# Performance work log

Measured on AMD Instinct MI355X. Metric: run time of the kernel, lower is better.

## Reference

```python
import jax, jax.numpy as jnp
import numpy as np

B, N, C, H = 2, 2048, 1024, 16
D = C // H  # head dim = 64


def setup_inputs() -> dict:
    key = jax.random.key(0)
    k1, k2, k3 = jax.random.split(key, 3)
    x = jax.random.normal(k1, (B, N, C), dtype=jnp.float32)
    w_qkv = jax.random.normal(k2, (C, 3 * C), dtype=jnp.float32) * 0.02
    w_proj = jax.random.normal(k3, (C, C), dtype=jnp.float32) * 0.02
    b_proj = jnp.zeros((C,), dtype=jnp.float32)
    return {"x": x, "w_qkv": w_qkv, "w_proj": w_proj, "b_proj": b_proj}


def reference(x, w_qkv, w_proj, b_proj):
    Bx, Nx, Cx = x.shape
    h, d = H, Cx // H
    # fused QKV projection (no bias: qkv_bias=False)
    qkv = x @ w_qkv  # [B, N, 3C]
    qkv = qkv.reshape(Bx, Nx, 3, h, d).transpose(2, 0, 3, 1, 4)  # [3, B, H, N, D]
    q, k, v = qkv[0], qkv[1], qkv[2]
    # scaled dot-product attention weights (full NxN matrix, as in flax)
    scale = jnp.asarray(1.0 / np.sqrt(d), dtype=x.dtype)
    scores = jnp.einsum('bhqd,bhkd->bhqk', q * scale, k)  # [B, H, N, N]
    attn = jax.nn.softmax(scores, axis=-1)
    # attention-value matmul, merge heads
    out = jnp.einsum('bhqk,bhkd->bhqd', attn, v)  # [B, H, N, D]
    out = out.swapaxes(1, 2).reshape(Bx, Nx, Cx)  # [B, N, C]
    # output projection (with bias: use_bias=True)
    return out @ w_proj + b_proj
```

## Files before the change

### kernel.cpp

```cpp
#include <hip/hip_runtime.h>
#include <cstdint>
#include <cstddef>

#define B_ 2
#define N_ 2048
#define C_ 1024
#define H_ 16

typedef unsigned short u16;
typedef __attribute__((ext_vector_type(8))) short bf16x8;
typedef __attribute__((ext_vector_type(4))) float f32x4;
typedef __attribute__((ext_vector_type(8))) u16 u16x8;
typedef __attribute__((ext_vector_type(4))) u16 u16x4;

static __device__ __forceinline__ u16 f2bf(float f) {
  unsigned int u = __builtin_bit_cast(unsigned int, f);
  u += 0x7FFFu + ((u >> 16) & 1u);
  return (u16)(u >> 16);
}

__global__ void cvt_f32_bf16(const float* __restrict__ in, u16* __restrict__ out) {
  const size_t i = (size_t)(blockIdx.x * blockDim.x + threadIdx.x) * 4;
  const float4 v = *(const float4*)(in + i);
  u16x4 o;
  o[0] = f2bf(v.x); o[1] = f2bf(v.y); o[2] = f2bf(v.z); o[3] = f2bf(v.w);
  *(u16x4*)(out + i) = o;
}

__global__ void tcvt_bf16(const float* __restrict__ in, u16* __restrict__ out,
                          int R, int Cn) {
  __shared__ float T[32][33];
  const int t = threadIdx.x;
  const int c0 = blockIdx.x * 32, r0 = blockIdx.y * 32;
  {
    const int r = t >> 3, c4 = (t & 7) * 4;
    const float4 v = *(const float4*)(in + (size_t)(r0 + r) * Cn + c0 + c4);
    T[r][c4 + 0] = v.x; T[r][c4 + 1] = v.y; T[r][c4 + 2] = v.z; T[r][c4 + 3] = v.w;
  }
  __syncthreads();
  {
    const int c = t >> 3, r4 = (t & 7) * 4;
    u16x4 o;
    o[0] = f2bf(T[r4 + 0][c]); o[1] = f2bf(T[r4 + 1][c]);
    o[2] = f2bf(T[r4 + 2][c]); o[3] = f2bf(T[r4 + 3][c]);
    *(u16x4*)(out + (size_t)(c0 + c) * R + r0 + r4) = o;
  }
}

__global__ __launch_bounds__(256, 4)
void vtrans(const u16* __restrict__ qkv, u16* __restrict__ vt) {
  __shared__ u16 T[64][72];
  const int tid = threadIdx.x;
  const int bh = blockIdx.x, tile = blockIdx.y;
  const int b = bh >> 4, h = bh & 15;
  const size_t src = (size_t)(b * N_ + tile * 64) * 3072 + 2048 + h * 64;
#pragma unroll
  for (int i = 0; i < 2; ++i) {
    const int f = tid + i * 256;
    const int row = f >> 3, d8 = (f & 7) * 8;
    *(u16x8*)&T[row][d8] = *(const u16x8*)(qkv + src + (size_t)row * 3072 + d8);
  }
  __syncthreads();
#pragma unroll
  for (int i = 0; i < 2; ++i) {
    const int f = tid + i * 256;
    const int d = f >> 3, n8 = (f & 7) * 8;
    u16x8 o;
#pragma unroll
    for (int j = 0; j < 8; ++j) o[j] = T[n8 + j][d];
    *(u16x8*)(vt + (size_t)(bh * 64 + d) * N_ + tile * 64 + n8) = o;
  }
}

template<bool BIAS, bool OUTBF>
__global__ __launch_bounds__(256, 2)
void gemm_bf16(const u16* __restrict__ A, const u16* __restrict__ Bt,
               const float* __restrict__ bias, float* __restrict__ Cf,
               u16* __restrict__ Cb, int M, int Nn, int K)
{
  __shared__ u16 As[128][40];
  __shared__ u16 Bs[128][40];

  const int tid = threadIdx.x;
  const int lane = tid & 63, wv = tid >> 6;
  const int wr = wv >> 1, wc = wv & 1;
  const int lr = lane & 15, lk = (lane >> 4) * 8;

  f32x4 acc[4][4];
#pragma unroll
  for (int m = 0; m < 4; ++m)
#pragma unroll
    for (int n = 0; n < 4; ++n) acc[m][n] = (f32x4){0.f, 0.f, 0.f, 0.f};

  const u16* Ag = A + (size_t)(blockIdx.y * 128) * K;
  const u16* Bg = Bt + (size_t)(blockIdx.x * 128) * K;

  for (int kt = 0; kt < K; kt += 32) {
#pragma unroll
    for (int i = 0; i < 2; ++i) {
      const int f = tid + i * 256;
      const int row = f >> 2, kq = (f & 3) * 8;
      *(u16x8*)&As[row][kq] = *(const u16x8*)(Ag + (size_t)row * K + kt + kq);
      *(u16x8*)&Bs[row][kq] = *(const u16x8*)(Bg + (size_t)row * K + kt + kq);
    }
    __syncthreads();

    bf16x8 a[4], b[4];
#pragma unroll
    for (int m = 0; m < 4; ++m) a[m] = *(bf16x8*)&As[wr * 64 + m * 16 + lr][lk];
#pragma unroll
    for (int n = 0; n < 4; ++n) b[n] = *(bf16x8*)&Bs[wc * 64 + n * 16 + lr][lk];
#pragma unroll
    for (int m = 0; m < 4; ++m)
#pragma unroll
      for (int n = 0; n < 4; ++n)
        acc[m][n] = __builtin_amdgcn_mfma_f32_16x16x32_bf16(a[m], b[n], acc[m][n], 0, 0, 0);
    __syncthreads();
  }

#pragma unroll
  for (int n = 0; n < 4; ++n) {
    const int col = blockIdx.x * 128 + wc * 64 + n * 16 + lr;
    const float bv = BIAS ? bias[col] : 0.f;
#pragma unroll
    for (int m = 0; m < 4; ++m) {
      const int rbase = blockIdx.y * 128 + wr * 64 + m * 16 + (lane >> 4) * 4;
#pragma unroll
      for (int r = 0; r < 4; ++r) {
        if (OUTBF) Cb[(size_t)(rbase + r) * Nn + col] = f2bf(acc[m][n][r]);
        else       Cf[(size_t)(rbase + r) * Nn + col] = acc[m][n][r] + bv;
      }
    }
  }
}

__global__ __launch_bounds__(256, 3)
void attn_mfma(const u16* __restrict__ qkv, const u16* __restrict__ vt,
               u16* __restrict__ att)
{
  __shared__ u16 Ks[64][72];
  __shared__ u16 Vs[64][72];
  __shared__ u16 Ps[64][72];

  const int tid = threadIdx.x;
  const int lane = tid & 63, wv = tid >> 6;
  const int l15 = lane & 15, lg = lane >> 4;
  const int qt = blockIdx.x;
  const int bh = blockIdx.y;
  const int b = bh >> 4, h = bh & 15;

  const size_t qbase = (size_t)(b * N_ + qt * 64) * 3072 + h * 64;
  const size_t kcol  = (size_t)b * N_ * 3072 + 1024 + h * 64;
  const size_t vbase = (size_t)(bh * 64) * N_;

#pragma unroll
  for (int i = 0; i < 2; ++i) {
    const int f = tid + i * 256;
    const int row = f >> 3, d8 = (f & 7) * 8;
    *(u16x8*)&Ps[row][d8] = *(const u16x8*)(qkv + qbase + (size_t)row * 3072 + d8);
  }
  __syncthreads();
  bf16x8 qf[2];
#pragma unroll
  for (int ks = 0; ks < 2; ++ks) qf[ks] = *(bf16x8*)&Ps[wv * 16 + l15][ks * 32 + lg * 8];
  __syncthreads();

  f32x4 accO[4];
#pragma unroll
  for (int n = 0; n < 4; ++n) accO[n] = (f32x4){0.f, 0.f, 0.f, 0.f};
  float m[4] = {-INFINITY, -INFINITY, -INFINITY, -INFINITY};
  float l[4] = {0.f, 0.f, 0.f, 0.f};

  for (int t = 0; t < N_ / 64; ++t) {
#pragma unroll
    for (int i = 0; i < 2; ++i) {
      const int f = tid + i * 256;
      const int row = f >> 3, c8 = (f & 7) * 8;
      *(u16x8*)&Ks[row][c8] =
          *(const u16x8*)(qkv + kcol + (size_t)(t * 64 + row) * 3072 + c8);
      *(u16x8*)&Vs[row][c8] =
          *(const u16x8*)(vt + vbase + (size_t)row * N_ + t * 64 + c8);
    }
    __syncthreads();

    f32x4 s[4];
#pragma unroll
    for (int n = 0; n < 4; ++n) {
      s[n] = (f32x4){0.f, 0.f, 0.f, 0.f};
#pragma unroll
      for (int ks = 0; ks < 2; ++ks) {
        const bf16x8 kf = *(bf16x8*)&Ks[n * 16 + l15][ks * 32 + lg * 8];
        s[n] = __builtin_amdgcn_mfma_f32_16x16x32_bf16(qf[ks], kf, s[n], 0, 0, 0);
      }
    }

    float mx[4], scf[4], ps[4];
#pragma unroll
    for (int n = 0; n < 4; ++n)
#pragma unroll
      for (int r = 0; r < 4; ++r) s[n][r] *= 0.125f;
#pragma unroll
    for (int r = 0; r < 4; ++r)
      mx[r] = fmaxf(fmaxf(s[0][r], s[1][r]), fmaxf(s[2][r], s[3][r]));
#pragma unroll
    for (int mask = 1; mask < 16; mask <<= 1)
#pragma unroll
      for (int r = 0; r < 4; ++r) mx[r] = fmaxf(mx[r], __shfl_xor(mx[r], mask));
#pragma unroll
    for (int r = 0; r < 4; ++r) {
      const float mn = fmaxf(m[r], mx[r]);
      scf[r] = __expf(m[r] - mn);
      m[r] = mn;
      ps[r] = 0.f;
    }
#pragma unroll
    for (int n = 0; n < 4; ++n)
#pragma unroll
      for (int r = 0; r < 4; ++r) {
        const float p = __expf(s[n][r] - m[r]);
        s[n][r] = p;
        ps[r] += p;
      }
#pragma unroll
    for (int mask = 1; mask < 16; mask <<= 1)
#pragma unroll
      for (int r = 0; r < 4; ++r) ps[r] += __shfl_xor(ps[r], mask);
#pragma unroll
    for (int r = 0; r < 4; ++r) l[r] = l[r] * scf[r] + ps[r];
#pragma unroll
    for (int n = 0; n < 4; ++n)
#pragma unroll
      for (int r = 0; r < 4; ++r) accO[n][r] *= scf[r];

#pragma unroll
    for (int n = 0; n < 4; ++n)
#pragma unroll
      for (int r = 0; r < 4; ++r)
        Ps[wv * 16 + lg * 4 + r][n * 16 + l15] = f2bf(s[n][r]);

#pragma unroll
    for (int ks = 0; ks < 2; ++ks) {
      const bf16x8 pa = *(bf16x8*)&Ps[wv * 16 + l15][ks * 32 + lg * 8];
#pragma unroll
      for (int n = 0; n < 4; ++n) {
        const bf16x8 vf = *(bf16x8*)&Vs[n * 16 + l15][ks * 32 + lg * 8];
        accO[n] = __builtin_amdgcn_mfma_f32_16x16x32_bf16(pa, vf, accO[n], 0, 0, 0);
      }
    }
    __syncthreads();
  }

  float inv[4];
#pragma unroll
  for (int r = 0; r < 4; ++r) inv[r] = 1.f / l[r];
#pragma unroll
  for (int n = 0; n < 4; ++n) {
    const int col = h * 64 + n * 16 + l15;
#pragma unroll
    for (int r = 0; r < 4; ++r) {
      const int row = b * N_ + qt * 64 + wv * 16 + lg * 4 + r;
      att[(size_t)row * C_ + col] = f2bf(accO[n][r] * inv[r]);
    }
  }
}

extern "C" void kernel_launch(void* const* d_in, const int* in_sizes, int n_in,
                              void* d_out, int out_size, void* d_ws, size_t ws_size,
                              hipStream_t stream) {
  const float* x      = (const float*)d_in[0];
  const float* w_qkv  = (const float*)d_in[1];
  const float* w_proj = (const float*)d_in[2];
  const float* b_proj = (const float*)d_in[3];
  float* out = (float*)d_out;

  u16* qkvb = (u16*)d_ws;
  u16* xb   = qkvb + (size_t)4096 * 3072;
  u16* wqt  = xb   + (size_t)4096 * 1024;
  u16* wpt  = wqt  + (size_t)3072 * 1024;
  u16* aob  = wpt  + (size_t)1024 * 1024;
  u16* vt   = xb;

  const int M = B_ * N_;

  cvt_f32_bf16<<<4096, 256, 0, stream>>>(x, xb);
  tcvt_bf16<<<dim3(96, 32), 256, 0, stream>>>(w_qkv, wqt, C_, 3 * C_);
  tcvt_bf16<<<dim3(32, 32), 256, 0, stream>>>(w_proj, wpt, C_, C_);

  gemm_bf16<false, true><<<dim3(3 * C_ / 128, M / 128), 256, 0, stream>>>(
      xb, wqt, nullptr, nullptr, qkvb, M, 3 * C_, C_);

  vtrans<<<dim3(32, 32), 256, 0, stream>>>(qkvb, vt);

  attn_mfma<<<dim3(N_ / 64, B_ * H_), 256, 0, stream>>>(qkvb, vt, aob);

  gemm_bf16<true, false><<<dim3(C_ / 128, M / 128), 256, 0, stream>>>(
      aob, wpt, b_proj, out, nullptr, M, C_, C_);
}
```

Baseline: 277.2 us.

## Double-buffer K/V tiles in attention and swizzle blocks for XCD locality

```diff
diff --git a/kernel.cpp b/kernel.cpp
--- a/kernel.cpp
+++ b/kernel.cpp
@@ -138,27 +138,32 @@
 void attn_mfma(const u16* __restrict__ qkv, const u16* __restrict__ vt,
                u16* __restrict__ att)
 {
-  __shared__ u16 Ks[64][72];
-  __shared__ u16 Vs[64][72];
+  __shared__ u16 Ks[2][64][72];
+  __shared__ u16 Vs[2][64][72];
   __shared__ u16 Ps[64][72];
 
   const int tid = threadIdx.x;
   const int lane = tid & 63, wv = tid >> 6;
   const int l15 = lane & 15, lg = lane >> 4;
-  const int qt = blockIdx.x;
-  const int bh = blockIdx.y;
+  const int bid = blockIdx.x;
+  const int swz = (bid & 7) * 128 + (bid >> 3);
+  const int bh = swz >> 5, qt = swz & 31;
   const int b = bh >> 4, h = bh & 15;
 
   const size_t qbase = (size_t)(b * N_ + qt * 64) * 3072 + h * 64;
   const size_t kcol  = (size_t)b * N_ * 3072 + 1024 + h * 64;
   const size_t vbase = (size_t)(bh * 64) * N_;
 
-#pragma unroll
-  for (int i = 0; i < 2; ++i) {
-    const int f = tid + i * 256;
-    const int row = f >> 3, d8 = (f & 7) * 8;
-    *(u16x8*)&Ps[row][d8] = *(const u16x8*)(qkv + qbase + (size_t)row * 3072 + d8);
-  }
+  const int f0 = tid, f1 = tid + 256;
+  const int row0 = f0 >> 3, c80 = (f0 & 7) * 8;
+  const int row1 = f1 >> 3, c81 = (f1 & 7) * 8;
+
+  *(u16x8*)&Ps[row0][c80] = *(const u16x8*)(qkv + qbase + (size_t)row0 * 3072 + c80);
+  *(u16x8*)&Ps[row1][c81] = *(const u16x8*)(qkv + qbase + (size_t)row1 * 3072 + c81);
+  *(u16x8*)&Ks[0][row0][c80] = *(const u16x8*)(qkv + kcol + (size_t)row0 * 3072 + c80);
+  *(u16x8*)&Ks[0][row1][c81] = *(const u16x8*)(qkv + kcol + (size_t)row1 * 3072 + c81);
+  *(u16x8*)&Vs[0][row0][c80] = *(const u16x8*)(vt + vbase + (size_t)row0 * N_ + c80);
+  *(u16x8*)&Vs[0][row1][c81] = *(const u16x8*)(vt + vbase + (size_t)row1 * N_ + c81);
   __syncthreads();
   bf16x8 qf[2];
 #pragma unroll
@@ -172,16 +177,16 @@
   float l[4] = {0.f, 0.f, 0.f, 0.f};
 
   for (int t = 0; t < N_ / 64; ++t) {
-#pragma unroll
-    for (int i = 0; i < 2; ++i) {
-      const int f = tid + i * 256;
-      const int row = f >> 3, c8 = (f & 7) * 8;
-      *(u16x8*)&Ks[row][c8] =
-          *(const u16x8*)(qkv + kcol + (size_t)(t * 64 + row) * 3072 + c8);
-      *(u16x8*)&Vs[row][c8] =
-          *(const u16x8*)(vt + vbase + (size_t)row * N_ + t * 64 + c8);
-    }
-    __syncthreads();
+    const int cur = t & 1;
+
+    u16x8 k0, k1, v0, v1;
+    if (t + 1 < N_ / 64) {
+      const size_t krow = kcol + (size_t)((t + 1) * 64) * 3072;
+      k0 = *(const u16x8*)(qkv + krow + (size_t)row0 * 3072 + c80);
+      k1 = *(const u16x8*)(qkv + krow + (size_t)row1 * 3072 + c81);
+      v0 = *(const u16x8*)(vt + vbase + (size_t)row0 * N_ + (t + 1) * 64 + c80);
+      v1 = *(const u16x8*)(vt + vbase + (size_t)row1 * N_ + (t + 1) * 64 + c81);
+    }
 
     f32x4 s[4];
 #pragma unroll
@@ -189,7 +194,7 @@
       s[n] = (f32x4){0.f, 0.f, 0.f, 0.f};
 #pragma unroll
       for (int ks = 0; ks < 2; ++ks) {
-        const bf16x8 kf = *(bf16x8*)&Ks[n * 16 + l15][ks * 32 + lg * 8];
+        const bf16x8 kf = *(bf16x8*)&Ks[cur][n * 16 + l15][ks * 32 + lg * 8];
         s[n] = __builtin_amdgcn_mfma_f32_16x16x32_bf16(qf[ks], kf, s[n], 0, 0, 0);
       }
     }
@@ -243,9 +248,16 @@
       const bf16x8 pa = *(bf16x8*)&Ps[wv * 16 + l15][ks * 32 + lg * 8];
 #pragma unroll
       for (int n = 0; n < 4; ++n) {
-        const bf16x8 vf = *(bf16x8*)&Vs[n * 16 + l15][ks * 32 + lg * 8];
+        const bf16x8 vf = *(bf16x8*)&Vs[cur][n * 16 + l15][ks * 32 + lg * 8];
         accO[n] = __builtin_amdgcn_mfma_f32_16x16x32_bf16(pa, vf, accO[n], 0, 0, 0);
       }
+    }
+
+    if (t + 1 < N_ / 64) {
+      *(u16x8*)&Ks[cur ^ 1][row0][c80] = k0;
+      *(u16x8*)&Ks[cur ^ 1][row1][c81] = k1;
+      *(u16x8*)&Vs[cur ^ 1][row0][c80] = v0;
+      *(u16x8*)&Vs[cur ^ 1][row1][c81] = v1;
     }
     __syncthreads();
   }
@@ -291,7 +303,7 @@
 
   vtrans<<<dim3(32, 32), 256, 0, stream>>>(qkvb, vt);
 
-  attn_mfma<<<dim3(N_ / 64, B_ * H_), 256, 0, stream>>>(qkvb, vt, aob);
+  attn_mfma<<<dim3(N_ / 64 * B_ * H_), 256, 0, stream>>>(qkvb, vt, aob);
 
   gemm_bf16<true, false><<<dim3(C_ / 128, M / 128), 256, 0, stream>>>(
       aob, wpt, b_proj, out, nullptr, M, C_, C_);
```

New measurement: 271.0 us. -2.2%, faster.
